# Optimization experiments

Measured on AMD Instinct MI355X. Metric: run time of the kernel, lower is better.

## Reference

```python
import jax, jax.numpy as jnp
import numpy as np

BETA = 0.25


def setup_inputs() -> dict:
    key = jax.random.key(0)
    k1, k2 = jax.random.split(key)
    B, C, H, W = 32, 64, 64, 64
    K = 1024
    z = jax.random.normal(k1, (B, C, H, W), dtype=jnp.float32)
    # nn.Embedding init: uniform(-1/K, 1/K)
    embedding = jax.random.uniform(k2, (K, C), dtype=jnp.float32,
                                   minval=-1.0 / K, maxval=1.0 / K)
    return {"z": z, "embedding": embedding}


def reference(z, embedding):
    B, C, H, W = z.shape
    z_hw_c = jnp.transpose(z, (0, 2, 3, 1))            # [B,H,W,C]
    z_flat = z_hw_c.reshape(-1, C)                      # [N,C], N=B*H*W
    # squared L2 distance: ||z||^2 + ||e||^2 - 2 z e^T
    d = (jnp.sum(z_flat ** 2, axis=1, keepdims=True)
         + jnp.sum(embedding ** 2, axis=1)
         - 2.0 * jnp.matmul(z_flat, embedding.T))       # [N,K]
    idx = jnp.argmin(d, axis=1)                         # [N]
    z_q = embedding[idx].reshape(z_hw_c.shape)          # [B,H,W,C]
    # commitment + codebook loss (detach emulated with stop_gradient)
    loss = (jnp.mean((jax.lax.stop_gradient(z_q) - z_hw_c) ** 2)
            + BETA * jnp.mean((z_q - jax.lax.stop_gradient(z_hw_c)) ** 2))
    # straight-through estimator
    z_q_st = z_hw_c + jax.lax.stop_gradient(z_q - z_hw_c)
    z_q_out = jnp.transpose(z_q_st, (0, 3, 1, 2))       # [B,C,H,W]
    min_encoding_indices = idx.reshape(B, H, W)
    return z_q_out, min_encoding_indices, loss
```

## Files before the change

### kernel.cpp

```cpp
#include <hip/hip_runtime.h>

#define C 64
#define K 1024
#define HW 4096
#define N_TOTAL 131072
#define OUT0 8388608
#define MT 128
#define KT 128
#define NTILES (K / KT)

#define WS_EK        0
#define WS_PARTIALS  1024
#define WS_BEST      3072
#define WS_NEED_FLOATS (3072 + N_TOTAL)

typedef unsigned int u32;
typedef unsigned long long u64;

__device__ __forceinline__ u64 packdk(float d, int k) {
    u32 b = __float_as_uint(d);
    u32 m = b ^ ((u32)((int)b >> 31) | 0x80000000u);
    return ((u64)m << 32) | (u32)k;
}

__global__ __launch_bounds__(256) void ek_kernel(const float* __restrict__ E,
                                                 float* __restrict__ ek) {
#pragma clang fp contract(off)
    int k = blockIdx.x * 256 + threadIdx.x;
    if (k >= K) return;
    const float* e = E + k * C;
    float r[8];
#pragma unroll
    for (int j = 0; j < 8; ++j) { float v = e[j]; r[j] = v * v; }
#pragma unroll
    for (int i = 8; i < C; i += 8) {
#pragma unroll
        for (int j = 0; j < 8; ++j) { float v = e[i + j]; r[j] += v * v; }
    }
    ek[k] = ((r[0] + r[1]) + (r[2] + r[3])) + ((r[4] + r[5]) + (r[6] + r[7]));
}

__global__ __launch_bounds__(256, 2) void vq_gemm(const float* __restrict__ Z,
                                                  const float* __restrict__ E,
                                                  const float* __restrict__ ek,
                                                  int* __restrict__ bestArr) {
#pragma clang fp contract(off)
    __shared__ float Zt[C * MT];
    __shared__ float Et[C * KT];
    __shared__ float znbuf[MT];
    __shared__ u64 red[4][8][8];

    const int t = threadIdx.x;
    const int n0 = blockIdx.x * MT;
    const int b = n0 >> 12;
    const int hw0 = n0 & 4095;
    const float* zbase = Z + b * (C * HW) + hw0;

#pragma unroll
    for (int r = 0; r < 8; ++r) {
        int idx4 = r * 256 + t;
        int c = idx4 >> 5, n4 = idx4 & 31;
        float4 v = *(const float4*)(zbase + c * HW + n4 * 4);
        *(float4*)(&Zt[c * MT + n4 * 4]) = v;
    }
    __syncthreads();

    if (t < MT) {
        float r8[8];
#pragma unroll
        for (int j = 0; j < 8; ++j) { float v = Zt[j * MT + t]; r8[j] = v * v; }
#pragma unroll
        for (int i = 1; i < 8; ++i)
#pragma unroll
            for (int j = 0; j < 8; ++j) { float v = Zt[(i * 8 + j) * MT + t]; r8[j] += v * v; }
        znbuf[t] = ((r8[0] + r8[1]) + (r8[2] + r8[3])) + ((r8[4] + r8[5]) + (r8[6] + r8[7]));
    }
    __syncthreads();

    const int wave = t >> 6, lane = t & 63;
    const int i_l = lane & 7, j_l = lane >> 3;
    const int ig = ((wave & 1) << 3) | i_l;
    const int jg = ((wave >> 1) << 3) | j_l;

    float znm[8];
#pragma unroll
    for (int m = 0; m < 8; ++m) znm[m] = znbuf[ig * 8 + m];

    u64 bestp[8];
#pragma unroll
    for (int m = 0; m < 8; ++m) bestp[m] = ~0ull;

    for (int tile = 0; tile < NTILES; ++tile) {
        __syncthreads();
        {
            int k_l = t & 127;
            int ch = t >> 7;
            const float* es = E + (tile * KT + k_l) * C + ch * 32;
#pragma unroll
            for (int r = 0; r < 8; ++r) {
                float4 v = *(const float4*)(es + r * 4);
                int c0 = ch * 32 + r * 4;
                Et[(c0 + 0) * KT + k_l] = v.x;
                Et[(c0 + 1) * KT + k_l] = v.y;
                Et[(c0 + 2) * KT + k_l] = v.z;
                Et[(c0 + 3) * KT + k_l] = v.w;
            }
        }
        __syncthreads();

        float ekq[8];
        {
            const float* ep = ek + tile * KT + jg * 8;
            float4 a = *(const float4*)ep;
            float4 bq = *(const float4*)(ep + 4);
            ekq[0] = a.x;  ekq[1] = a.y;  ekq[2] = a.z;  ekq[3] = a.w;
            ekq[4] = bq.x; ekq[5] = bq.y; ekq[6] = bq.z; ekq[7] = bq.w;
        }

        float acc[8][8];
#pragma unroll
        for (int m = 0; m < 8; ++m)
#pragma unroll
            for (int q = 0; q < 8; ++q) acc[m][q] = 0.0f;

#pragma unroll 8
        for (int c = 0; c < C; ++c) {
            float4 za = *(const float4*)(&Zt[c * MT + ig * 8]);
            float4 zb = *(const float4*)(&Zt[c * MT + ig * 8 + 4]);
            float4 ea = *(const float4*)(&Et[c * KT + jg * 8]);
            float4 eb = *(const float4*)(&Et[c * KT + jg * 8 + 4]);
            float zm[8] = {za.x, za.y, za.z, za.w, zb.x, zb.y, zb.z, zb.w};
            float eq[8] = {ea.x, ea.y, ea.z, ea.w, eb.x, eb.y, eb.z, eb.w};
#pragma unroll
            for (int m = 0; m < 8; ++m)
#pragma unroll
                for (int q = 0; q < 8; ++q)
                    acc[m][q] = __builtin_fmaf(zm[m], eq[q], acc[m][q]);
        }

#pragma unroll
        for (int m = 0; m < 8; ++m)
#pragma unroll
            for (int q = 0; q < 8; ++q) {
                float A = znm[m] + ekq[q];
                float d = A - 2.0f * acc[m][q];
                u64 p = packdk(d, tile * KT + jg * 8 + q);
                if (p < bestp[m]) bestp[m] = p;
            }
    }

#pragma unroll
    for (int m = 0; m < 8; ++m) {
        u64 v = bestp[m];
#pragma unroll
        for (int mask = 8; mask <= 32; mask <<= 1) {
            u64 o = __shfl_xor(v, mask, 64);
            v = o < v ? o : v;
        }
        bestp[m] = v;
    }
    if (j_l == 0) {
#pragma unroll
        for (int m = 0; m < 8; ++m) red[wave][i_l][m] = bestp[m];
    }
    __syncthreads();
    if (t < MT) {
        int igg = t >> 3, m = t & 7;
        int ihalf = igg >> 3, iw = igg & 7;
        u64 a = red[ihalf][iw][m];
        u64 b2 = red[ihalf + 2][iw][m];
        u64 v = b2 < a ? b2 : a;
        bestArr[n0 + t] = (int)(v & 0xFFFFFFFFu);
    }
}

__global__ __launch_bounds__(256) void vq_epilogue(const float* __restrict__ Z,
                                                   const float* __restrict__ E,
                                                   const int* __restrict__ bestArr,
                                                   float* __restrict__ out,
                                                   float* __restrict__ partials) {
#pragma clang fp contract(off)
    int n = blockIdx.x * 256 + threadIdx.x;
    int b = n >> 12;
    int hw = n & 4095;
    int best = bestArr[n];

    const float* zp = Z + b * (C * HW) + hw;
    const float4* eb4 = (const float4*)(E + best * C);
    float* o0 = out + b * (C * HW) + hw;
    float ls = 0.0f;
#pragma unroll
    for (int c4 = 0; c4 < 16; ++c4) {
        float4 e4 = eb4[c4];
        int cb = c4 * 4;
        float z0 = zp[(cb + 0) * HW], z1 = zp[(cb + 1) * HW];
        float z2 = zp[(cb + 2) * HW], z3 = zp[(cb + 3) * HW];
        float f0 = e4.x - z0; o0[(cb + 0) * HW] = z0 + f0; ls += f0 * f0;
        float f1 = e4.y - z1; o0[(cb + 1) * HW] = z1 + f1; ls += f1 * f1;
        float f2 = e4.z - z2; o0[(cb + 2) * HW] = z2 + f2; ls += f2 * f2;
        float f3 = e4.w - z3; o0[(cb + 3) * HW] = z3 + f3; ls += f3 * f3;
    }
    out[OUT0 + n] = (float)best;

#pragma unroll
    for (int off = 32; off > 0; off >>= 1) ls += __shfl_xor(ls, off, 64);
    if ((threadIdx.x & 63) == 0) partials[n >> 6] = ls;
}

__global__ __launch_bounds__(256, 4) void vq_combined(const float* __restrict__ Z,
                                                      const float* __restrict__ E,
                                                      const float* __restrict__ ek,
                                                      float* __restrict__ out,
                                                      float* __restrict__ partials) {
#pragma clang fp contract(off)
    int n = blockIdx.x * 256 + threadIdx.x;
    int b = n >> 12;
    int hw = n & 4095;
    const float* zp = Z + b * (C * HW) + hw;

    float z[C];
#pragma unroll
    for (int c = 0; c < C; ++c) z[c] = zp[c * HW];
    float zn;
    {
        float r[8];
#pragma unroll
        for (int j = 0; j < 8; ++j) r[j] = z[j] * z[j];
#pragma unroll
        for (int i = 8; i < C; i += 8) {
#pragma unroll
            for (int j = 0; j < 8; ++j) r[j] += z[i + j] * z[i + j];
        }
        zn = ((r[0] + r[1]) + (r[2] + r[3])) + ((r[4] + r[5]) + (r[6] + r[7]));
    }

    float dmin = __builtin_inff();
    int best = 0;
#pragma unroll 1
    for (int k = 0; k < K; k += 4) {
        const float* e0 = E + k * C;
        float a0 = 0.0f, a1 = 0.0f, a2 = 0.0f, a3 = 0.0f;
#pragma unroll
        for (int c = 0; c < C; ++c) {
            float zc = z[c];
            a0 = __builtin_fmaf(zc, e0[c], a0);
            a1 = __builtin_fmaf(zc, e0[C + c], a1);
            a2 = __builtin_fmaf(zc, e0[2 * C + c], a2);
            a3 = __builtin_fmaf(zc, e0[3 * C + c], a3);
        }
        float A0 = zn + ek[k],     A1 = zn + ek[k + 1];
        float A2 = zn + ek[k + 2], A3 = zn + ek[k + 3];
        float d0 = A0 - 2.0f * a0, d1 = A1 - 2.0f * a1;
        float d2 = A2 - 2.0f * a2, d3 = A3 - 2.0f * a3;
        if (d0 < dmin) { dmin = d0; best = k; }
        if (d1 < dmin) { dmin = d1; best = k + 1; }
        if (d2 < dmin) { dmin = d2; best = k + 2; }
        if (d3 < dmin) { dmin = d3; best = k + 3; }
    }

    const float4* eb4 = (const float4*)(E + best * C);
    float* o0 = out + b * (C * HW) + hw;
    float ls = 0.0f;
#pragma unroll
    for (int c4 = 0; c4 < 16; ++c4) {
        float4 e4 = eb4[c4];
        int cb = c4 * 4;
        float f0 = e4.x - z[cb + 0]; o0[(cb + 0) * HW] = z[cb + 0] + f0; ls += f0 * f0;
        float f1 = e4.y - z[cb + 1]; o0[(cb + 1) * HW] = z[cb + 1] + f1; ls += f1 * f1;
        float f2 = e4.z - z[cb + 2]; o0[(cb + 2) * HW] = z[cb + 2] + f2; ls += f2 * f2;
        float f3 = e4.w - z[cb + 3]; o0[(cb + 3) * HW] = z[cb + 3] + f3; ls += f3 * f3;
    }
    out[OUT0 + n] = (float)best;
#pragma unroll
    for (int off = 32; off > 0; off >>= 1) ls += __shfl_xor(ls, off, 64);
    if ((threadIdx.x & 63) == 0) partials[n >> 6] = ls;
}

__global__ __launch_bounds__(256) void loss_kernel(const float* __restrict__ partials,
                                                   float* __restrict__ out) {
    __shared__ double sm[256];
    int t = threadIdx.x;
    double s = 0.0;
    for (int i = t; i < (N_TOTAL / 64); i += 256) s += (double)partials[i];
    sm[t] = s;
    __syncthreads();
    for (int o = 128; o > 0; o >>= 1) {
        if (t < o) sm[t] += sm[t + o];
        __syncthreads();
    }
    if (t == 0) {
        float m = (float)(sm[0] * (1.0 / 8388608.0));
        float loss = m + 0.25f * m;
        out[OUT0 + N_TOTAL] = loss;
    }
}

extern "C" void kernel_launch(void* const* d_in, const int* in_sizes, int n_in,
                              void* d_out, int out_size, void* d_ws, size_t ws_size,
                              hipStream_t stream) {
    const float* Z = (const float*)d_in[0];
    const float* E = (const float*)d_in[1];
    float* out = (float*)d_out;
    float* ws = (float*)d_ws;
    float* ek = ws + WS_EK;
    float* partials = ws + WS_PARTIALS;

    hipLaunchKernelGGL(ek_kernel, dim3(4), dim3(256), 0, stream, E, ek);

    if (ws_size >= (size_t)WS_NEED_FLOATS * sizeof(float)) {
        int* bestArr = (int*)(ws + WS_BEST);
        hipLaunchKernelGGL(vq_gemm, dim3(N_TOTAL / MT), dim3(256), 0, stream,
                           Z, E, ek, bestArr);
        hipLaunchKernelGGL(vq_epilogue, dim3(N_TOTAL / 256), dim3(256), 0, stream,
                           Z, E, bestArr, out, partials);
    } else {
        hipLaunchKernelGGL(vq_combined, dim3(N_TOTAL / 256), dim3(256), 0, stream,
                           Z, E, ek, out, partials);
    }
    hipLaunchKernelGGL(loss_kernel, dim3(1), dim3(256), 0, stream, partials, out);
}
```

Baseline: 249.2 us.

## Fuse VQ GEMM with epilogue and read pre-transposed codebook from global memory

A prep kernel now computes codebook norms and writes a channel-major transposed copy of the codebook to workspace. The main kernel reads codebook tiles straight from that copy (L2/cache resident) instead of staging them in shared memory, which removes the per-tile barriers and LDS transposes. The argmin tracks a float minimum plus index instead of packed 64-bit compares, and the gather, output and loss epilogue is fused into the same kernel using the Z tile already in shared memory. This drops one kernel and the index round trip. The risks are higher global load latency in the inner loop, and only half the threads doing the epilogue work.

```diff
diff --git a/kernel.cpp b/kernel.cpp
--- a/kernel.cpp
+++ b/kernel.cpp
@@ -11,8 +11,8 @@
 
 #define WS_EK        0
 #define WS_PARTIALS  1024
-#define WS_BEST      3072
-#define WS_NEED_FLOATS (3072 + N_TOTAL)
+#define WS_ETG       3072
+#define WS_NEED_FLOATS (3072 + C * K)
 
 typedef unsigned int u32;
 typedef unsigned long long u64;
@@ -21,6 +21,182 @@
     u32 b = __float_as_uint(d);
     u32 m = b ^ ((u32)((int)b >> 31) | 0x80000000u);
     return ((u64)m << 32) | (u32)k;
+}
+
+__global__ __launch_bounds__(256) void eprep_kernel(const float* __restrict__ E,
+                                                    float* __restrict__ Etg,
+                                                    float* __restrict__ ek) {
+#pragma clang fp contract(off)
+    int k = blockIdx.x * 256 + threadIdx.x;
+    const float* e = E + k * C;
+    float ev[C];
+#pragma unroll
+    for (int c4 = 0; c4 < 16; ++c4) {
+        float4 v = *(const float4*)(e + c4 * 4);
+        ev[c4 * 4 + 0] = v.x; ev[c4 * 4 + 1] = v.y;
+        ev[c4 * 4 + 2] = v.z; ev[c4 * 4 + 3] = v.w;
+    }
+    float r[8];
+#pragma unroll
+    for (int j = 0; j < 8; ++j) r[j] = ev[j] * ev[j];
+#pragma unroll
+    for (int i = 8; i < C; i += 8)
+#pragma unroll
+        for (int j = 0; j < 8; ++j) r[j] += ev[i + j] * ev[i + j];
+    ek[k] = ((r[0] + r[1]) + (r[2] + r[3])) + ((r[4] + r[5]) + (r[6] + r[7]));
+#pragma unroll
+    for (int c = 0; c < C; ++c) Etg[c * K + k] = ev[c];
+}
+
+__global__ __launch_bounds__(256, 4) void vq_main(const float* __restrict__ Z,
+                                                  const float* __restrict__ E,
+                                                  const float* __restrict__ Etg,
+                                                  const float* __restrict__ ek,
+                                                  float* __restrict__ out,
+                                                  float* __restrict__ partials) {
+#pragma clang fp contract(off)
+    __shared__ float Zt[C * MT];
+    __shared__ float znbuf[MT];
+    __shared__ u64 red[4][8][8];
+
+    const int t = threadIdx.x;
+    const int n0 = blockIdx.x * MT;
+    const int b = n0 >> 12;
+    const int hw0 = n0 & 4095;
+    const float* zbase = Z + b * (C * HW) + hw0;
+
+#pragma unroll
+    for (int r = 0; r < 8; ++r) {
+        int idx4 = r * 256 + t;
+        int c = idx4 >> 5, n4 = idx4 & 31;
+        float4 v = *(const float4*)(zbase + c * HW + n4 * 4);
+        *(float4*)(&Zt[c * MT + n4 * 4]) = v;
+    }
+    __syncthreads();
+
+    if (t < MT) {
+        float r8[8];
+#pragma unroll
+        for (int j = 0; j < 8; ++j) { float v = Zt[j * MT + t]; r8[j] = v * v; }
+#pragma unroll
+        for (int i = 1; i < 8; ++i)
+#pragma unroll
+            for (int j = 0; j < 8; ++j) { float v = Zt[(i * 8 + j) * MT + t]; r8[j] += v * v; }
+        znbuf[t] = ((r8[0] + r8[1]) + (r8[2] + r8[3])) + ((r8[4] + r8[5]) + (r8[6] + r8[7]));
+    }
+    __syncthreads();
+
+    const int wave = t >> 6, lane = t & 63;
+    const int i_l = lane & 7, j_l = lane >> 3;
+    const int ig = ((wave & 1) << 3) | i_l;
+    const int jg = ((wave >> 1) << 3) | j_l;
+
+    float znm[8];
+#pragma unroll
+    for (int m = 0; m < 8; ++m) znm[m] = znbuf[ig * 8 + m];
+
+    float dmin[8];
+    int qb[8];
+#pragma unroll
+    for (int m = 0; m < 8; ++m) { dmin[m] = __builtin_inff(); qb[m] = 0; }
+
+    const float* ep = Etg + jg * 8;
+
+#pragma unroll 1
+    for (int tile = 0; tile < NTILES; ++tile) {
+        float ekq[8];
+        {
+            const float* ekp = ek + tile * KT + jg * 8;
+            float4 a = *(const float4*)ekp;
+            float4 bq = *(const float4*)(ekp + 4);
+            ekq[0] = a.x;  ekq[1] = a.y;  ekq[2] = a.z;  ekq[3] = a.w;
+            ekq[4] = bq.x; ekq[5] = bq.y; ekq[6] = bq.z; ekq[7] = bq.w;
+        }
+
+        float acc[8][8];
+#pragma unroll
+        for (int m = 0; m < 8; ++m)
+#pragma unroll
+            for (int q = 0; q < 8; ++q) acc[m][q] = 0.0f;
+
+        const float* ept = ep + tile * KT;
+#pragma unroll 8
+        for (int c = 0; c < C; ++c) {
+            float4 za = *(const float4*)(&Zt[c * MT + ig * 8]);
+            float4 zb = *(const float4*)(&Zt[c * MT + ig * 8 + 4]);
+            float4 ea = *(const float4*)(ept + c * K);
+            float4 eb = *(const float4*)(ept + c * K + 4);
+            float zm[8] = {za.x, za.y, za.z, za.w, zb.x, zb.y, zb.z, zb.w};
+            float eq[8] = {ea.x, ea.y, ea.z, ea.w, eb.x, eb.y, eb.z, eb.w};
+#pragma unroll
+            for (int m = 0; m < 8; ++m)
+#pragma unroll
+                for (int q = 0; q < 8; ++q)
+                    acc[m][q] = __builtin_fmaf(zm[m], eq[q], acc[m][q]);
+        }
+
+        const int qbase = tile * 8;
+#pragma unroll
+        for (int m = 0; m < 8; ++m)
+#pragma unroll
+            for (int q = 0; q < 8; ++q) {
+                float A = znm[m] + ekq[q];
+                float d = __builtin_fmaf(-2.0f, acc[m][q], A);
+                if (d < dmin[m]) { dmin[m] = d; qb[m] = qbase + q; }
+            }
+    }
+
+    u64 bestp[8];
+#pragma unroll
+    for (int m = 0; m < 8; ++m) {
+        int q8 = qb[m];
+        int k = ((q8 >> 3) << 7) + jg * 8 + (q8 & 7);
+        bestp[m] = packdk(dmin[m], k);
+    }
+#pragma unroll
+    for (int m = 0; m < 8; ++m) {
+        u64 v = bestp[m];
+#pragma unroll
+        for (int mask = 8; mask <= 32; mask <<= 1) {
+            u64 o = __shfl_xor(v, mask, 64);
+            v = o < v ? o : v;
+        }
+        bestp[m] = v;
+    }
+    if (j_l == 0) {
+#pragma unroll
+        for (int m = 0; m < 8; ++m) red[wave][i_l][m] = bestp[m];
+    }
+    __syncthreads();
+
+    if (t < MT) {
+        int igg = t >> 3, m = t & 7;
+        int ihalf = igg >> 3, iw = igg & 7;
+        u64 a = red[ihalf][iw][m];
+        u64 b2 = red[ihalf + 2][iw][m];
+        u64 v = b2 < a ? b2 : a;
+        int best = (int)(v & 0xFFFFFFFFu);
+        int n = n0 + t;
+        out[OUT0 + n] = (float)best;
+
+        const float4* eb4 = (const float4*)(E + best * C);
+        float* o0 = out + b * (C * HW) + hw0 + t;
+        float ls = 0.0f;
+#pragma unroll
+        for (int c4 = 0; c4 < 16; ++c4) {
+            float4 e4 = eb4[c4];
+            int cb = c4 * 4;
+            float z0 = Zt[(cb + 0) * MT + t], z1 = Zt[(cb + 1) * MT + t];
+            float z2 = Zt[(cb + 2) * MT + t], z3 = Zt[(cb + 3) * MT + t];
+            float f0 = e4.x - z0; o0[(cb + 0) * HW] = z0 + f0; ls += f0 * f0;
+            float f1 = e4.y - z1; o0[(cb + 1) * HW] = z1 + f1; ls += f1 * f1;
+            float f2 = e4.z - z2; o0[(cb + 2) * HW] = z2 + f2; ls += f2 * f2;
+            float f3 = e4.w - z3; o0[(cb + 3) * HW] = z3 + f3; ls += f3 * f3;
+        }
+#pragma unroll
+        for (int off = 32; off > 0; off >>= 1) ls += __shfl_xor(ls, off, 64);
+        if ((t & 63) == 0) partials[n >> 6] = ls;
+    }
 }
 
 __global__ __launch_bounds__(256) void ek_kernel(const float* __restrict__ E,
@@ -38,173 +214,6 @@
         for (int j = 0; j < 8; ++j) { float v = e[i + j]; r[j] += v * v; }
     }
     ek[k] = ((r[0] + r[1]) + (r[2] + r[3])) + ((r[4] + r[5]) + (r[6] + r[7]));
-}
-
-__global__ __launch_bounds__(256, 2) void vq_gemm(const float* __restrict__ Z,
-                                                  const float* __restrict__ E,
-                                                  const float* __restrict__ ek,
-                                                  int* __restrict__ bestArr) {
-#pragma clang fp contract(off)
-    __shared__ float Zt[C * MT];
-    __shared__ float Et[C * KT];
-    __shared__ float znbuf[MT];
-    __shared__ u64 red[4][8][8];
-
-    const int t = threadIdx.x;
-    const int n0 = blockIdx.x * MT;
-    const int b = n0 >> 12;
-    const int hw0 = n0 & 4095;
-    const float* zbase = Z + b * (C * HW) + hw0;
-
-#pragma unroll
-    for (int r = 0; r < 8; ++r) {
-        int idx4 = r * 256 + t;
-        int c = idx4 >> 5, n4 = idx4 & 31;
-        float4 v = *(const float4*)(zbase + c * HW + n4 * 4);
-        *(float4*)(&Zt[c * MT + n4 * 4]) = v;
-    }
-    __syncthreads();
-
-    if (t < MT) {
-        float r8[8];
-#pragma unroll
-        for (int j = 0; j < 8; ++j) { float v = Zt[j * MT + t]; r8[j] = v * v; }
-#pragma unroll
-        for (int i = 1; i < 8; ++i)
-#pragma unroll
-            for (int j = 0; j < 8; ++j) { float v = Zt[(i * 8 + j) * MT + t]; r8[j] += v * v; }
-        znbuf[t] = ((r8[0] + r8[1]) + (r8[2] + r8[3])) + ((r8[4] + r8[5]) + (r8[6] + r8[7]));
-    }
-    __syncthreads();
-
-    const int wave = t >> 6, lane = t & 63;
-    const int i_l = lane & 7, j_l = lane >> 3;
-    const int ig = ((wave & 1) << 3) | i_l;
-    const int jg = ((wave >> 1) << 3) | j_l;
-
-    float znm[8];
-#pragma unroll
-    for (int m = 0; m < 8; ++m) znm[m] = znbuf[ig * 8 + m];
-
-    u64 bestp[8];
-#pragma unroll
-    for (int m = 0; m < 8; ++m) bestp[m] = ~0ull;
-
-    for (int tile = 0; tile < NTILES; ++tile) {
-        __syncthreads();
-        {
-            int k_l = t & 127;
-            int ch = t >> 7;
-            const float* es = E + (tile * KT + k_l) * C + ch * 32;
-#pragma unroll
-            for (int r = 0; r < 8; ++r) {
-                float4 v = *(const float4*)(es + r * 4);
-                int c0 = ch * 32 + r * 4;
-                Et[(c0 + 0) * KT + k_l] = v.x;
-                Et[(c0 + 1) * KT + k_l] = v.y;
-                Et[(c0 + 2) * KT + k_l] = v.z;
-                Et[(c0 + 3) * KT + k_l] = v.w;
-            }
-        }
-        __syncthreads();
-
-        float ekq[8];
-        {
-            const float* ep = ek + tile * KT + jg * 8;
-            float4 a = *(const float4*)ep;
-            float4 bq = *(const float4*)(ep + 4);
-            ekq[0] = a.x;  ekq[1] = a.y;  ekq[2] = a.z;  ekq[3] = a.w;
-            ekq[4] = bq.x; ekq[5] = bq.y; ekq[6] = bq.z; ekq[7] = bq.w;
-        }
-
-        float acc[8][8];
-#pragma unroll
-        for (int m = 0; m < 8; ++m)
-#pragma unroll
-            for (int q = 0; q < 8; ++q) acc[m][q] = 0.0f;
-
-#pragma unroll 8
-        for (int c = 0; c < C; ++c) {
-            float4 za = *(const float4*)(&Zt[c * MT + ig * 8]);
-            float4 zb = *(const float4*)(&Zt[c * MT + ig * 8 + 4]);
-            float4 ea = *(const float4*)(&Et[c * KT + jg * 8]);
-            float4 eb = *(const float4*)(&Et[c * KT + jg * 8 + 4]);
-            float zm[8] = {za.x, za.y, za.z, za.w, zb.x, zb.y, zb.z, zb.w};
-            float eq[8] = {ea.x, ea.y, ea.z, ea.w, eb.x, eb.y, eb.z, eb.w};
-#pragma unroll
-            for (int m = 0; m < 8; ++m)
-#pragma unroll
-                for (int q = 0; q < 8; ++q)
-                    acc[m][q] = __builtin_fmaf(zm[m], eq[q], acc[m][q]);
-        }
-
-#pragma unroll
-        for (int m = 0; m < 8; ++m)
-#pragma unroll
-            for (int q = 0; q < 8; ++q) {
-                float A = znm[m] + ekq[q];
-                float d = A - 2.0f * acc[m][q];
-                u64 p = packdk(d, tile * KT + jg * 8 + q);
-                if (p < bestp[m]) bestp[m] = p;
-            }
-    }
-
-#pragma unroll
-    for (int m = 0; m < 8; ++m) {
-        u64 v = bestp[m];
-#pragma unroll
-        for (int mask = 8; mask <= 32; mask <<= 1) {
-            u64 o = __shfl_xor(v, mask, 64);
-            v = o < v ? o : v;
-        }
-        bestp[m] = v;
-    }
-    if (j_l == 0) {
-#pragma unroll
-        for (int m = 0; m < 8; ++m) red[wave][i_l][m] = bestp[m];
-    }
-    __syncthreads();
-    if (t < MT) {
-        int igg = t >> 3, m = t & 7;
-        int ihalf = igg >> 3, iw = igg & 7;
-        u64 a = red[ihalf][iw][m];
-        u64 b2 = red[ihalf + 2][iw][m];
-        u64 v = b2 < a ? b2 : a;
-        bestArr[n0 + t] = (int)(v & 0xFFFFFFFFu);
-    }
-}
-
-__global__ __launch_bounds__(256) void vq_epilogue(const float* __restrict__ Z,
-                                                   const float* __restrict__ E,
-                                                   const int* __restrict__ bestArr,
-                                                   float* __restrict__ out,
-                                                   float* __restrict__ partials) {
-#pragma clang fp contract(off)
-    int n = blockIdx.x * 256 + threadIdx.x;
-    int b = n >> 12;
-    int hw = n & 4095;
-    int best = bestArr[n];
-
-    const float* zp = Z + b * (C * HW) + hw;
-    const float4* eb4 = (const float4*)(E + best * C);
-    float* o0 = out + b * (C * HW) + hw;
-    float ls = 0.0f;
-#pragma unroll
-    for (int c4 = 0; c4 < 16; ++c4) {
-        float4 e4 = eb4[c4];
-        int cb = c4 * 4;
-        float z0 = zp[(cb + 0) * HW], z1 = zp[(cb + 1) * HW];
-        float z2 = zp[(cb + 2) * HW], z3 = zp[(cb + 3) * HW];
-        float f0 = e4.x - z0; o0[(cb + 0) * HW] = z0 + f0; ls += f0 * f0;
-        float f1 = e4.y - z1; o0[(cb + 1) * HW] = z1 + f1; ls += f1 * f1;
-        float f2 = e4.z - z2; o0[(cb + 2) * HW] = z2 + f2; ls += f2 * f2;
-        float f3 = e4.w - z3; o0[(cb + 3) * HW] = z3 + f3; ls += f3 * f3;
-    }
-    out[OUT0 + n] = (float)best;
-
-#pragma unroll
-    for (int off = 32; off > 0; off >>= 1) ls += __shfl_xor(ls, off, 64);
-    if ((threadIdx.x & 63) == 0) partials[n >> 6] = ls;
 }
 
 __global__ __launch_bounds__(256, 4) void vq_combined(const float* __restrict__ Z,
@@ -305,15 +314,14 @@
     float* ek = ws + WS_EK;
     float* partials = ws + WS_PARTIALS;
 
-    hipLaunchKernelGGL(ek_kernel, dim3(4), dim3(256), 0, stream, E, ek);
-
     if (ws_size >= (size_t)WS_NEED_FLOATS * sizeof(float)) {
-        int* bestArr = (int*)(ws + WS_BEST);
-        hipLaunchKernelGGL(vq_gemm, dim3(N_TOTAL / MT), dim3(256), 0, stream,
-                           Z, E, ek, bestArr);
-        hipLaunchKernelGGL(vq_epilogue, dim3(N_TOTAL / 256), dim3(256), 0, stream,
-                           Z, E, bestArr, out, partials);
+        float* Etg = ws + WS_ETG;
+        hipLaunchKernelGGL(eprep_kernel, dim3(K / 256), dim3(256), 0, stream,
+                           E, Etg, ek);
+        hipLaunchKernelGGL(vq_main, dim3(N_TOTAL / MT), dim3(256), 0, stream,
+                           Z, E, Etg, ek, out, partials);
     } else {
+        hipLaunchKernelGGL(ek_kernel, dim3(4), dim3(256), 0, stream, E, ek);
         hipLaunchKernelGGL(vq_combined, dim3(N_TOTAL / 256), dim3(256), 0, stream,
                            Z, E, ek, out, partials);
     }
```

Measured after the change: 272.0 us. +9.2%, slower.
